# Kernel tuning notes

Measured on AMD Instinct MI355X. Metric: run time of the kernel, lower is better.

Reference implementation:

```python
import jax, jax.numpy as jnp
import numpy as np

B, S, D, H = 4, 2048, 1024, 16
HD = D // H
FF = 4 * D
EPS = 1e-5


def _layer_norm(x, w, b):
    mu = jnp.mean(x, axis=-1, keepdims=True)
    var = jnp.mean(jnp.square(x - mu), axis=-1, keepdims=True)
    return (x - mu) * jax.lax.rsqrt(var + EPS) * w + b


def setup_inputs() -> dict:
    key = jax.random.key(0)
    ks = jax.random.split(key, 8)
    std = 0.02
    return {
        "x": jax.random.normal(ks[0], (B, S, D), dtype=jnp.float32),
        "ln1_w": jnp.ones((D,), jnp.float32),
        "ln1_b": jnp.zeros((D,), jnp.float32),
        "w_qkv": jax.random.normal(ks[1], (D, 3 * D), dtype=jnp.float32) * std,  # fused QKV, no bias
        "w_proj": jax.random.normal(ks[2], (D, D), dtype=jnp.float32) * std,
        "b_proj": jnp.zeros((D,), jnp.float32),
        "ln2_w": jnp.ones((D,), jnp.float32),
        "ln2_b": jnp.zeros((D,), jnp.float32),
        "w_ff1": jax.random.normal(ks[3], (D, FF), dtype=jnp.float32) * std,
        "b_ff1": jnp.zeros((FF,), jnp.float32),
        "w_ff2": jax.random.normal(ks[4], (FF, D), dtype=jnp.float32) * std,
        "b_ff2": jnp.zeros((D,), jnp.float32),
    }


def reference(x, ln1_w, ln1_b, w_qkv, w_proj, b_proj, ln2_w, ln2_b, w_ff1, b_ff1, w_ff2, b_ff2):
    b, s, d = x.shape
    # --- attention branch (pre-LN) ---
    h = _layer_norm(x, ln1_w, ln1_b)
    kqv = (h @ w_qkv).reshape(b, s, H, HD, 3)  # fused projection, split by last index
    k, q, v = kqv[..., 0], kqv[..., 1], kqv[..., 2]  # each [b, s, H, HD]
    scores = jnp.einsum("bqhd,bkhd->bhqk", q, k) * (HD ** -0.5)  # [b,H,s,s]
    causal = jnp.tril(jnp.ones((s, s), dtype=bool))
    scores = jnp.where(causal, scores, -jnp.inf)
    weights = jax.nn.softmax(scores, axis=-1)
    ctx = jnp.einsum("bhqk,bkhd->bqhd", weights, v).reshape(b, s, d)
    attn_out = ctx @ w_proj + b_proj
    x = x + attn_out
    # --- feed-forward branch (pre-LN) ---
    h = _layer_norm(x, ln2_w, ln2_b)
    ff = jax.nn.gelu(h @ w_ff1 + b_ff1, approximate=False) @ w_ff2 + b_ff2
    return x + ff
```

## Files before the change

### kernel.cpp

```cpp
#include <hip/hip_runtime.h>

typedef unsigned short u16;
typedef unsigned int u32;
typedef __bf16 bf16x8 __attribute__((ext_vector_type(8)));
typedef float f32x4 __attribute__((ext_vector_type(4)));
typedef float f32x16 __attribute__((ext_vector_type(16)));
typedef unsigned short us8 __attribute__((ext_vector_type(8)));
typedef unsigned short us4 __attribute__((ext_vector_type(4)));
typedef unsigned int u32x4 __attribute__((ext_vector_type(4)));

#define B_ 4
#define S_ 2048
#define D_ 1024
#define H_ 16
#define HD_ 64
#define EPS_ 1e-5f
#define SCALE_ (0.125f * 1.44269504088896341f)
#define THR_ 3.0f

__device__ __forceinline__ u16 f2bf(float f) {
  unsigned u = __builtin_bit_cast(unsigned, f);
  u = (u + 0x7FFFu + ((u >> 16) & 1u)) >> 16;
  return (u16)u;
}

__device__ __forceinline__ float gelu_f(float x) {
  float u = x * (2.3022388f + 0.10294971f * x * x);
  float te = __builtin_amdgcn_exp2f(u);
  return x - x * __builtin_amdgcn_rcpf(1.0f + te);
}

typedef const __attribute__((address_space(1))) unsigned int* gp1;
typedef __attribute__((address_space(3))) unsigned int* lp3;
__device__ __forceinline__ void gl_lds16(const void* g, void* l) {
  __builtin_amdgcn_global_load_lds((gp1)(unsigned long long)g,
                                   (lp3)(unsigned int)(unsigned long long)l,
                                   16, 0, 0);
}

__device__ __forceinline__ u32 cvtpk_bf16(float lo, float hi) {
  u32 d;
  asm("v_cvt_pk_bf16_f32 %0, %1, %2" : "=v"(d) : "v"(lo), "v"(hi));
  return d;
}
__device__ __forceinline__ void swap32(u32& a, u32& b) {
  asm("v_permlane32_swap_b32 %0, %1" : "+v"(a), "+v"(b));
}

__device__ __forceinline__ f32x16 zero16() {
  f32x16 z;
#pragma unroll
  for (int i = 0; i < 16; i++) z[i] = 0.f;
  return z;
}

__global__ __launch_bounds__(256) void wconv_kernel(const float* __restrict__ W,
                                                    u16* __restrict__ Wt,
                                                    int Kd, int N) {
  __shared__ u16 tile[32][33];
  int bid = blockIdx.x;
  int nbn = N >> 5;
  int tk = bid / nbn, tn = bid % nbn;
  int tx = threadIdx.x & 31, ty = threadIdx.x >> 5;
#pragma unroll
  for (int i = 0; i < 4; i++) {
    int r = ty + i * 8;
    tile[r][tx] = f2bf(W[(size_t)(tk * 32 + r) * N + tn * 32 + tx]);
  }
  __syncthreads();
#pragma unroll
  for (int i = 0; i < 4; i++) {
    int r = ty + i * 8;
    Wt[(size_t)(tn * 32 + r) * Kd + tk * 32 + tx] = tile[tx][r];
  }
}

__global__ __launch_bounds__(256) void vtrans_kernel(const u16* __restrict__ Vc,
                                                     u16* __restrict__ Vt) {
  __shared__ u16 tile[64][72];
  int bh = blockIdx.x >> 5;
  int sb = blockIdx.x & 31;
  const u16* src = Vc + ((size_t)bh * S_ + sb * 64) * HD_;
  int r = threadIdx.x >> 2, c0 = (threadIdx.x & 3) * 16;
  *(us8*)&tile[r][c0] = *(const us8*)(src + r * HD_ + c0);
  *(us8*)&tile[r][c0 + 8] = *(const us8*)(src + r * HD_ + c0 + 8);
  __syncthreads();
  u16* dst = Vt + (size_t)bh * HD_ * S_ + sb * 64;
  int hd = threadIdx.x >> 2;
  int s0 = (threadIdx.x & 3) * 16;
  us8 a, b;
#pragma unroll
  for (int j = 0; j < 8; j++) a[j] = tile[s0 + j][hd];
#pragma unroll
  for (int j = 0; j < 8; j++) b[j] = tile[s0 + 8 + j][hd];
  *(us8*)(dst + (size_t)hd * S_ + s0) = a;
  *(us8*)(dst + (size_t)hd * S_ + s0 + 8) = b;
}

__global__ __launch_bounds__(256) void ln_kernel(const float* __restrict__ x,
                                                 const float* __restrict__ w,
                                                 const float* __restrict__ b,
                                                 u16* __restrict__ out) {
  int row = blockIdx.x;
  int t = threadIdx.x;
  int lane = t & 63, wid = t >> 6;
  const float4* xr = (const float4*)(x + (size_t)row * D_);
  float4 v = xr[t];
  float s = v.x + v.y + v.z + v.w;
  float q = v.x * v.x + v.y * v.y + v.z * v.z + v.w * v.w;
#pragma unroll
  for (int off = 1; off < 64; off <<= 1) {
    s += __shfl_xor(s, off);
    q += __shfl_xor(q, off);
  }
  __shared__ float red[8];
  if (lane == 0) { red[wid] = s; red[4 + wid] = q; }
  __syncthreads();
  s = red[0] + red[1] + red[2] + red[3];
  q = red[4] + red[5] + red[6] + red[7];
  float mu = s * (1.0f / D_);
  float var = q * (1.0f / D_) - mu * mu;
  float rs = rsqrtf(var + EPS_);
  int c = t * 4;
  float4 wv = *(const float4*)(w + c);
  float4 bv = *(const float4*)(b + c);
  us4 o;
  o[0] = f2bf((v.x - mu) * rs * wv.x + bv.x);
  o[1] = f2bf((v.y - mu) * rs * wv.y + bv.y);
  o[2] = f2bf((v.z - mu) * rs * wv.z + bv.z);
  o[3] = f2bf((v.w - mu) * rs * wv.w + bv.w);
  *(us4*)(out + (size_t)row * D_ + c) = o;
}

#define VWAIT(n)                                              \
  do {                                                        \
    asm volatile("s_waitcnt vmcnt(" #n ")" ::: "memory");     \
    __builtin_amdgcn_sched_barrier(0);                        \
  } while (0)

#define LDA(AF, MQ)                                                             \
  _Pragma("unroll") for (int ks = 0; ks < 2; ks++) {                            \
    int slot = ((((ks << 2) | lgr) ^ sl7)) * 8;                                 \
    _Pragma("unroll") for (int m = 0; m < MH; m++)                              \
      AF[ks][m] = *(const bf16x8*)&Ac[((MQ) * (BM / 2) + wm * (BM / 4) +        \
                                       m * 16 + lrow) * 64 + slot];             \
  }

#define LDB(BF, NQ)                                                             \
  _Pragma("unroll") for (int ks = 0; ks < 2; ks++) {                            \
    int slot = ((((ks << 2) | lgr) ^ sl7)) * 8;                                 \
    _Pragma("unroll") for (int nn = 0; nn < 2; nn++)                            \
      BF[ks][nn] = *(const bf16x8*)&Bc[((NQ) * 128 + wn * 32 + nn * 16 +        \
                                        lrow) * 64 + slot];                     \
  }

#define BARR_MFMA(MQ, NQ, AF, BF)                                               \
  __builtin_amdgcn_s_barrier();                                                 \
  asm volatile("s_waitcnt lgkmcnt(0)" ::: "memory");                            \
  __builtin_amdgcn_sched_barrier(0);                                            \
  __builtin_amdgcn_s_setprio(1);                                                \
  _Pragma("unroll") for (int m = 0; m < MH; m++)                                \
    _Pragma("unroll") for (int nn = 0; nn < 2; nn++) {                          \
      acc[MQ][NQ][m][nn] = __builtin_amdgcn_mfma_f32_16x16x32_bf16(             \
          AF[0][m], BF[0][nn], acc[MQ][NQ][m][nn], 0, 0, 0);                    \
      acc[MQ][NQ][m][nn] = __builtin_amdgcn_mfma_f32_16x16x32_bf16(             \
          AF[1][m], BF[1][nn], acc[MQ][NQ][m][nn], 0, 0, 0);                    \
    }                                                                           \
  __builtin_amdgcn_s_setprio(0);                                                \
  __builtin_amdgcn_s_barrier();                                                 \
  __builtin_amdgcn_sched_barrier(0);

template <int MODE, int BM>
__global__ __launch_bounds__(512) void gemm8p_kernel(
    const u16* __restrict__ A, const u16* __restrict__ Bt,
    const float* __restrict__ bias, const float* __restrict__ res,
    float* __restrict__ Cf, u16* __restrict__ Cb,
    u16* __restrict__ Qc, u16* __restrict__ Kc, u16* __restrict__ Vc,
    int M, int N, int K) {
  constexpr int LA = BM / 128;
  constexpr int MH = BM / 64;
  constexpr int ASZ = BM * 64;
  constexpr int BSZ = 256 * 64;
  extern __shared__ __align__(16) u16 sm[];
  int t = threadIdx.x;
  int nbn = N >> 8;
  int nwg = gridDim.x, cpx = nwg >> 3;
  int bid = (blockIdx.x % 8) * cpx + blockIdx.x / 8;
  int bm = bid / nbn, bn = bid % nbn;
  int lane = t & 63, wid = t >> 6;
  int wm = wid >> 2, wn = wid & 3;
  int lrow = lane & 15, lgr = lane >> 4;
  int sl7 = lrow & 7;
  const u16* Ab = A + (size_t)bm * BM * K;
  const u16* Bb = Bt + (size_t)bn * 256 * K;
  int srt = t >> 3;
  int ssc = (((t & 7) ^ (srt & 7)) << 3);
  const u16* Asrc = Ab + (size_t)srt * K + ssc;
  const u16* Bsrc = Bb + (size_t)srt * K + ssc;

  auto stageA = [&](int kt, int bsel, int h) {
    int k0 = kt * 64;
    u16* dst = sm + bsel * (ASZ + BSZ) + (h * (BM / 2)) * 64 + t * 8;
#pragma unroll
    for (int a = 0; a < LA; a++)
      gl_lds16(Asrc + (size_t)(h * (BM / 2) + a * 64) * K + k0, dst + a * 4096);
  };
  auto stageB = [&](int kt, int bsel, int h) {
    int k0 = kt * 64;
    u16* dst = sm + bsel * (ASZ + BSZ) + ASZ + (h * 128) * 64 + t * 8;
#pragma unroll
    for (int b2 = 0; b2 < 2; b2++)
      gl_lds16(Bsrc + (size_t)(h * 128 + b2 * 64) * K + k0, dst + b2 * 4096);
  };

  f32x4 acc[2][2][MH][2] = {};
  int NT = K >> 6;
  stageA(0, 0, 0);
  stageB(0, 0, 0);
  stageB(0, 0, 1);
  stageA(0, 0, 1);
  if constexpr (BM == 256) VWAIT(4); else VWAIT(3);
  __builtin_amdgcn_s_barrier();
  __builtin_amdgcn_sched_barrier(0);
  for (int kt = 0; kt < NT - 1; kt++) {
    int cur = kt & 1, nb = cur ^ 1;
    const u16* Ac = sm + cur * (ASZ + BSZ);
    const u16* Bc = Ac + ASZ;
    bf16x8 af[2][MH], bf[2][2];
    LDA(af, 0);
    LDB(bf, 0);
    stageA(kt + 1, nb, 0);
    if constexpr (BM == 256) VWAIT(4); else VWAIT(2);
    BARR_MFMA(0, 0, af, bf);
    LDB(bf, 1);
    stageB(kt + 1, nb, 0);
    if constexpr (BM == 256) VWAIT(4); else VWAIT(3);
    BARR_MFMA(0, 1, af, bf);
    LDA(af, 1);
    stageB(kt + 1, nb, 1);
    BARR_MFMA(1, 1, af, bf);
    LDB(bf, 0);
    stageA(kt + 1, nb, 1);
    if constexpr (BM == 256) VWAIT(4); else VWAIT(3);
    BARR_MFMA(1, 0, af, bf);
  }
  {
    int cur = (NT - 1) & 1;
    const u16* Ac = sm + cur * (ASZ + BSZ);
    const u16* Bc = Ac + ASZ;
    bf16x8 af[2][MH], bf[2][2];
    LDA(af, 0);
    LDB(bf, 0);
    if constexpr (BM == 256) VWAIT(2); else VWAIT(1);
    BARR_MFMA(0, 0, af, bf);
    LDB(bf, 1);
    VWAIT(0);
    BARR_MFMA(0, 1, af, bf);
    LDA(af, 1);
    BARR_MFMA(1, 1, af, bf);
    LDB(bf, 0);
    BARR_MFMA(1, 0, af, bf);
  }
#pragma unroll
  for (int nq = 0; nq < 2; nq++) {
#pragma unroll
    for (int nn = 0; nn < 2; nn++) {
      int col = bn * 256 + nq * 128 + wn * 32 + nn * 16 + lrow;
      float bv = (MODE & 1) ? bias[col] : 0.0f;
      if (MODE & 16) {
        int c = col % 3;
        int hd = (col / 3) & 63;
        int h = col / 192;
        u16* dst = (c == 0) ? Kc : (c == 1) ? Qc : Vc;
#pragma unroll
        for (int mq = 0; mq < 2; mq++)
#pragma unroll
          for (int m = 0; m < MH; m++)
#pragma unroll
            for (int r = 0; r < 4; r++) {
              int row = bm * BM + mq * (BM / 2) + wm * (BM / 4) + m * 16 + lgr * 4 + r;
              int bb = row >> 11, sIdx = row & 2047;
              dst[(((size_t)(bb * H_ + h)) * S_ + sIdx) * HD_ + hd] =
                  f2bf(acc[mq][nq][m][nn][r]);
            }
      } else {
#pragma unroll
        for (int mq = 0; mq < 2; mq++)
#pragma unroll
          for (int m = 0; m < MH; m++)
#pragma unroll
            for (int r = 0; r < 4; r++) {
              int row = bm * BM + mq * (BM / 2) + wm * (BM / 4) + m * 16 + lgr * 4 + r;
              float v = acc[mq][nq][m][nn][r] + bv;
              if (MODE & 2) v = gelu_f(v);
              if (MODE & 4) v += res[(size_t)row * N + col];
              if (MODE & 8) Cb[(size_t)row * N + col] = f2bf(v);
              else          Cf[(size_t)row * N + col] = v;
            }
      }
    }
  }
}

__device__ __forceinline__ void attn_softmax_update(
    f32x16* s, int NSUB_rt, float& mrun, float& lrun, f32x16 (&o)[2], int hi) {
  float pmax = -3.0e38f;
  for (int sub = 0; sub < NSUB_rt; sub++)
#pragma unroll
    for (int r = 0; r < 16; r++) pmax = fmaxf(pmax, s[sub][r]);
  pmax = fmaxf(pmax, __shfl_xor(pmax, 32));
  bool ok = (pmax * SCALE_ <= mrun + THR_);
  if (!__all(ok)) {
    float mnew = fmaxf(mrun, pmax * SCALE_);
    float corr = __builtin_amdgcn_exp2f(mrun - mnew);
    mrun = mnew;
    lrun *= corr;
#pragma unroll
    for (int r = 0; r < 16; r++) {
      float cr = __shfl(corr, ((r & 3) + 8 * (r >> 2)) + 4 * hi);
      o[0][r] *= cr;
      o[1][r] *= cr;
    }
  }
  float m = mrun;
  float lacc = 0.f;
  for (int sub = 0; sub < NSUB_rt; sub++)
#pragma unroll
    for (int r = 0; r < 16; r++) {
      float p = __builtin_amdgcn_exp2f(__builtin_fmaf(s[sub][r], SCALE_, -m));
      s[sub][r] = p;
      lacc += p;
    }
  lrun += lacc;
}

__device__ __forceinline__ void attn_pfrag(const f32x16& s, bf16x8& pa, bf16x8& pb) {
  u32 a0 = cvtpk_bf16(s[0], s[1]);
  u32 a1 = cvtpk_bf16(s[2], s[3]);
  u32 a2 = cvtpk_bf16(s[4], s[5]);
  u32 a3 = cvtpk_bf16(s[6], s[7]);
  swap32(a0, a2);
  swap32(a1, a3);
  u32 b0 = cvtpk_bf16(s[8], s[9]);
  u32 b1 = cvtpk_bf16(s[10], s[11]);
  u32 b2 = cvtpk_bf16(s[12], s[13]);
  u32 b3 = cvtpk_bf16(s[14], s[15]);
  swap32(b0, b2);
  swap32(b1, b3);
  u32x4 fa = {a0, a1, a2, a3};
  u32x4 fb = {b0, b1, b2, b3};
  pa = __builtin_bit_cast(bf16x8, fa);
  pb = __builtin_bit_cast(bf16x8, fb);
}

template <bool MASK>
__device__ __forceinline__ void attn_chunk_tail(
    const u16* __restrict__ Kh, const u16* __restrict__ Vh,
    const bf16x8 (&qf)[4], f32x16 (&o)[2],
    float& mrun, float& lrun, int kb, int qrow, int hi, int ln31) {
  f32x16 s[1];
  f32x16 z = zero16();
  __builtin_amdgcn_s_setprio(1);
#pragma unroll
  for (int ks = 0; ks < 4; ks++) {
    bf16x8 kfr = *(const bf16x8*)(Kh + (size_t)(kb + ln31) * HD_ + ks * 16 + hi * 8);
    z = __builtin_amdgcn_mfma_f32_32x32x16_bf16(kfr, qf[ks], z, 0, 0, 0);
  }
  __builtin_amdgcn_s_setprio(0);
  if (MASK) {
#pragma unroll
    for (int r = 0; r < 16; r++) {
      int key = kb + (r & 3) + 8 * (r >> 2) + 4 * hi;
      if (key > qrow) z[r] = -3.0e38f;
    }
  }
  s[0] = z;
  attn_softmax_update(s, 1, mrun, lrun, o, hi);
  bf16x8 pa, pb;
  attn_pfrag(s[0], pa, pb);
  __builtin_amdgcn_s_setprio(1);
#pragma unroll
  for (int ht = 0; ht < 2; ht++) {
    const u16* vb = Vh + (size_t)(ht * 32 + ln31) * S_ + kb + hi * 8;
    bf16x8 v1 = *(const bf16x8*)(vb);
    bf16x8 v2 = *(const bf16x8*)(vb + 16);
    o[ht] = __builtin_amdgcn_mfma_f32_32x32x16_bf16(pa, v1, o[ht], 0, 0, 0);
    o[ht] = __builtin_amdgcn_mfma_f32_32x32x16_bf16(pb, v2, o[ht], 0, 0, 0);
  }
  __builtin_amdgcn_s_setprio(0);
}

__global__ __launch_bounds__(512) void attn_kernel(const u16* __restrict__ Q,
                                                   const u16* __restrict__ Kk,
                                                   const u16* __restrict__ Vt,
                                                   u16* __restrict__ ctx) {
  __shared__ __align__(16) u16 Kl[2][64 * 64];
  __shared__ __align__(16) u16 Vl[2][64 * 64];
  int t = threadIdx.x;
  int lane = t & 63, wid = t >> 6;
  int qblk = 7 - (int)(blockIdx.x >> 6);
  int bh = blockIdx.x & 63;
  int b = bh >> 4, h = bh & 15;
  const u16* Qh = Q + (size_t)bh * S_ * HD_;
  const u16* Kh = Kk + (size_t)bh * S_ * HD_;
  const u16* Vh = Vt + (size_t)bh * HD_ * S_;
  int qb = qblk * 256;
  int qbase = qb + wid * 32;
  int ln31 = lane & 31, hi = lane >> 5;
  int qrow = qbase + ln31;
  int l7 = ln31 & 7;

  int srow = t >> 3;
  int sslot = (t & 7) ^ (srow & 7);
  const u16* Ksrc = Kh + (size_t)srow * HD_ + sslot * 8;
  const u16* Vsrc = Vh + (size_t)srow * S_ + sslot * 8;

  bf16x8 qf[4];
#pragma unroll
  for (int ks = 0; ks < 4; ks++)
    qf[ks] = *(const bf16x8*)(Qh + (size_t)qrow * HD_ + ks * 16 + hi * 8);

  f32x16 o[2] = {zero16(), zero16()};
  float mrun = -1.0e30f, lrun = 0.f;

  int nf64 = qbase >> 6;
  int NT = (qb >> 6) + 3;

  gl_lds16(Ksrc, &Kl[0][t * 8]);
  gl_lds16(Vsrc, &Vl[0][t * 8]);
  for (int kt = 0; kt < NT; kt++) {
    int cur = kt & 1;
    if (kt + 1 < NT) {
      int kb1 = (kt + 1) * 64;
      gl_lds16(Ksrc + (size_t)kb1 * HD_, &Kl[cur ^ 1][t * 8]);
      gl_lds16(Vsrc + kb1, &Vl[cur ^ 1][t * 8]);
      asm volatile("s_waitcnt vmcnt(2)" ::: "memory");
    } else {
      asm volatile("s_waitcnt vmcnt(0)" ::: "memory");
    }
    __builtin_amdgcn_sched_barrier(0);
    __builtin_amdgcn_s_barrier();
    __builtin_amdgcn_sched_barrier(0);
    if (kt < nf64) {
      const u16* Kc = &Kl[cur][0];
      const u16* Vc = &Vl[cur][0];
      f32x16 s[2];
#pragma unroll
      for (int sub = 0; sub < 2; sub++) {
        f32x16 z = zero16();
        __builtin_amdgcn_s_setprio(1);
#pragma unroll
        for (int ks = 0; ks < 4; ks++) {
          int kr = sub * 32 + ln31;
          int sl = (ks * 2 + hi) ^ l7;
          bf16x8 kfr = *(const bf16x8*)&Kc[kr * 64 + sl * 8];
          z = __builtin_amdgcn_mfma_f32_32x32x16_bf16(kfr, qf[ks], z, 0, 0, 0);
        }
        __builtin_amdgcn_s_setprio(0);
        s[sub] = z;
      }
      attn_softmax_update(s, 2, mrun, lrun, o, hi);
#pragma unroll
      for (int sub = 0; sub < 2; sub++) {
        bf16x8 pa, pb;
        attn_pfrag(s[sub], pa, pb);
        __builtin_amdgcn_s_setprio(1);
#pragma unroll
        for (int ht = 0; ht < 2; ht++) {
          int vr = ht * 32 + ln31;
          int s1 = (sub * 4 + hi) ^ (vr & 7);
          int s2 = (sub * 4 + hi + 2) ^ (vr & 7);
          bf16x8 v1 = *(const bf16x8*)&Vc[vr * 64 + s1 * 8];
          bf16x8 v2 = *(const bf16x8*)&Vc[vr * 64 + s2 * 8];
          o[ht] = __builtin_amdgcn_mfma_f32_32x32x16_bf16(pa, v1, o[ht], 0, 0, 0);
          o[ht] = __builtin_amdgcn_mfma_f32_32x32x16_bf16(pb, v2, o[ht], 0, 0, 0);
        }
        __builtin_amdgcn_s_setprio(0);
      }
    }
    __builtin_amdgcn_sched_barrier(0);
    __builtin_amdgcn_s_barrier();
    __builtin_amdgcn_sched_barrier(0);
  }

  if (qbase & 32)
    attn_chunk_tail<false>(Kh, Vh, qf, o, mrun, lrun, qbase - 32, qrow, hi, ln31);
  attn_chunk_tail<true>(Kh, Vh, qf, o, mrun, lrun, qbase, qrow, hi, ln31);

  float l = lrun + __shfl_xor(lrun, 32);
  float inv = 1.0f / l;
#pragma unroll
  for (int r = 0; r < 16; r++) {
    float invr = __shfl(inv, ((r & 3) + 8 * (r >> 2)) + 4 * hi);
    int q = qbase + (r & 3) + 8 * (r >> 2) + 4 * hi;
    size_t base = ((size_t)b * S_ + q) * D_ + h * HD_;
    ctx[base + ln31] = f2bf(o[0][r] * invr);
    ctx[base + 32 + ln31] = f2bf(o[1][r] * invr);
  }
}

extern "C" void kernel_launch(void* const* d_in, const int* in_sizes, int n_in,
                              void* d_out, int out_size, void* d_ws, size_t ws_size,
                              hipStream_t stream) {
  const float* x = (const float*)d_in[0];
  const float* ln1w = (const float*)d_in[1];
  const float* ln1b = (const float*)d_in[2];
  const float* wqkv = (const float*)d_in[3];
  const float* wproj = (const float*)d_in[4];
  const float* bproj = (const float*)d_in[5];
  const float* ln2w = (const float*)d_in[6];
  const float* ln2b = (const float*)d_in[7];
  const float* wff1 = (const float*)d_in[8];
  const float* bff1 = (const float*)d_in[9];
  const float* wff2 = (const float*)d_in[10];
  const float* bff2 = (const float*)d_in[11];

  char* ws = (char*)d_ws;
  u16* wqkvT = (u16*)(ws + 0);
  u16* wprojT = (u16*)(ws + 6291456);
  u16* wff1T = (u16*)(ws + 8388608);
  u16* wff2T = (u16*)(ws + 16777216);
  u16* h1 = (u16*)(ws + 25165824);
  u16* Vt = (u16*)(ws + 25165824);
  u16* Qc = (u16*)(ws + 41943040);
  u16* Kc = (u16*)(ws + 58720256);
  u16* Vc = (u16*)(ws + 75497472);
  u16* ctx = (u16*)(ws + 92274688);
  float* x1 = (float*)(ws + 109051904);
  u16* h2 = (u16*)(ws + 142606336);
  u16* g = (u16*)(ws + 25165824);
  float* outp = (float*)d_out;

  hipFuncSetAttribute((const void*)gemm8p_kernel<16, 256>,
                      hipFuncAttributeMaxDynamicSharedMemorySize, 131072);
  hipFuncSetAttribute((const void*)gemm8p_kernel<11, 256>,
                      hipFuncAttributeMaxDynamicSharedMemorySize, 131072);
  hipFuncSetAttribute((const void*)gemm8p_kernel<5, 128>,
                      hipFuncAttributeMaxDynamicSharedMemorySize, 98304);

  wconv_kernel<<<(1024 / 32) * (3072 / 32), 256, 0, stream>>>(wqkv, wqkvT, 1024, 3072);
  wconv_kernel<<<(1024 / 32) * (1024 / 32), 256, 0, stream>>>(wproj, wprojT, 1024, 1024);
  wconv_kernel<<<(1024 / 32) * (4096 / 32), 256, 0, stream>>>(wff1, wff1T, 1024, 4096);
  wconv_kernel<<<(4096 / 32) * (1024 / 32), 256, 0, stream>>>(wff2, wff2T, 4096, 1024);

  ln_kernel<<<8192, 256, 0, stream>>>(x, ln1w, ln1b, h1);
  gemm8p_kernel<16, 256><<<384, 512, 131072, stream>>>(h1, wqkvT, nullptr, nullptr,
                                                       nullptr, nullptr, Qc, Kc, Vc,
                                                       8192, 3072, 1024);
  vtrans_kernel<<<64 * 32, 256, 0, stream>>>(Vc, Vt);
  attn_kernel<<<8 * 64, 512, 0, stream>>>(Qc, Kc, Vt, ctx);
  gemm8p_kernel<5, 128><<<256, 512, 98304, stream>>>(ctx, wprojT, bproj, x, x1, nullptr,
                                                     nullptr, nullptr, nullptr,
                                                     8192, 1024, 1024);
  ln_kernel<<<8192, 256, 0, stream>>>(x1, ln2w, ln2b, h2);
  gemm8p_kernel<11, 256><<<512, 512, 131072, stream>>>(h2, wff1T, bff1, nullptr, nullptr, g,
                                                       nullptr, nullptr, nullptr,
                                                       8192, 4096, 1024);
  gemm8p_kernel<5, 128><<<256, 512, 98304, stream>>>(g, wff2T, bff2, x1, outp, nullptr,
                                                     nullptr, nullptr, nullptr,
                                                     8192, 1024, 4096);
}
```

Baseline: 379.1 us.

## Deepen GEMM global-to-LDS prefetch to stage halves two tiles ahead

Restructures the GEMM main loop so that some A/B half-tiles are prefetched two k-steps ahead into the buffer being consumed, while the rest come one step ahead. The peeled last iteration is folded into the loop with guards. Wait counts are raised to match. The goal is to hide more global-load latency behind MFMA work. It risks races on the reused LDS buffer and adds per-iteration branches.

```diff
diff --git a/kernel.cpp b/kernel.cpp
--- a/kernel.cpp
+++ b/kernel.cpp
@@ -219,46 +219,36 @@
   stageB(0, 0, 0);
   stageB(0, 0, 1);
   stageA(0, 0, 1);
+  stageA(1, 1, 0);
+  stageB(1, 1, 1);
   if constexpr (BM == 256) VWAIT(4); else VWAIT(3);
   __builtin_amdgcn_s_barrier();
   __builtin_amdgcn_sched_barrier(0);
-  for (int kt = 0; kt < NT - 1; kt++) {
+  for (int kt = 0; kt < NT; kt++) {
     int cur = kt & 1, nb = cur ^ 1;
     const u16* Ac = sm + cur * (ASZ + BSZ);
     const u16* Bc = Ac + ASZ;
     bf16x8 af[2][MH], bf[2][2];
     LDA(af, 0);
     LDB(bf, 0);
-    stageA(kt + 1, nb, 0);
-    if constexpr (BM == 256) VWAIT(4); else VWAIT(2);
+    if (kt + 1 < NT) stageB(kt + 1, nb, 0);
     BARR_MFMA(0, 0, af, bf);
     LDB(bf, 1);
-    stageB(kt + 1, nb, 0);
-    if constexpr (BM == 256) VWAIT(4); else VWAIT(3);
+    if (kt + 1 < NT) stageA(kt + 1, nb, 1);
+    if (kt == NT - 1) { VWAIT(0); }
+    else if constexpr (BM == 256) { VWAIT(8); }
+    else { VWAIT(6); }
     BARR_MFMA(0, 1, af, bf);
     LDA(af, 1);
-    stageB(kt + 1, nb, 1);
+    if (kt + 2 < NT) stageA(kt + 2, cur, 0);
     BARR_MFMA(1, 1, af, bf);
     LDB(bf, 0);
-    stageA(kt + 1, nb, 1);
-    if constexpr (BM == 256) VWAIT(4); else VWAIT(3);
-    BARR_MFMA(1, 0, af, bf);
-  }
-  {
-    int cur = (NT - 1) & 1;
-    const u16* Ac = sm + cur * (ASZ + BSZ);
-    const u16* Bc = Ac + ASZ;
-    bf16x8 af[2][MH], bf[2][2];
-    LDA(af, 0);
-    LDB(bf, 0);
-    if constexpr (BM == 256) VWAIT(2); else VWAIT(1);
-    BARR_MFMA(0, 0, af, bf);
-    LDB(bf, 1);
-    VWAIT(0);
-    BARR_MFMA(0, 1, af, bf);
-    LDA(af, 1);
-    BARR_MFMA(1, 1, af, bf);
-    LDB(bf, 0);
+    if (kt + 2 < NT) stageB(kt + 2, cur, 1);
+    if (kt + 2 < NT) {
+      if constexpr (BM == 256) { VWAIT(6); } else { VWAIT(4); }
+    } else if (kt + 1 < NT) {
+      if constexpr (BM == 256) { VWAIT(2); } else { VWAIT(1); }
+    }
     BARR_MFMA(1, 0, af, bf);
   }
 #pragma unroll
```

Result: slower. 404.9 us (+6.8%).
